# Kernel tuning notes

Hardware: AMD Instinct MI355X
Metric: run time of the kernel (lower is better)

Reference implementation:

```python
import jax, jax.numpy as jnp
import numpy as np

B_SZ, N_IN, N_CTX, UNITS, RANK = 4096, 4096, 512, 4096, 256


def setup_inputs() -> dict:
    key = jax.random.key(0)
    ks = jax.random.split(key, 8)
    inputs = jax.random.normal(ks[0], (B_SZ, N_IN), dtype=jnp.float32)
    context = jax.random.normal(ks[1], (B_SZ, N_CTX), dtype=jnp.float32)
    # Orthogonal-ish init approximated by scaled normals (math-equivalent shapes)
    U = jax.random.normal(ks[2], (N_IN, RANK), dtype=jnp.float32) / np.sqrt(N_IN)
    S = jax.random.uniform(ks[3], (RANK,), dtype=jnp.float32, minval=0.5, maxval=1.5)
    V = jax.random.normal(ks[4], (UNITS, RANK), dtype=jnp.float32) / np.sqrt(UNITS)
    W = jax.random.normal(ks[5], (N_CTX, RANK), dtype=jnp.float32) / np.sqrt(N_CTX)
    B = jnp.zeros((RANK,), dtype=jnp.float32)
    bias = jnp.zeros((UNITS,), dtype=jnp.float32)
    return {"inputs": inputs, "context": context, "U": U, "S": S, "V": V, "W": W, "B": B, "bias": bias}


def reference(inputs, context, U, S, V, W, B, bias):
    # chi[b,r] = sigmoid(context @ W + B)
    chi = jax.nn.sigmoid(context @ W + B)                  # [B, R]
    # Original: kernel[b,n,m] = sum_r U[n,r]*S[r]*chi[b,r]*V[m,r];
    # out[b,m] = sum_n x[b,n]*kernel[b,n,m]. Algebraically equal to:
    t = (inputs @ U) * (S * chi)                           # [B, R]
    out = t @ V.T + bias                                   # first '+ self.bias'
    out = out + bias                                       # 'outputs += self.bias' (use_bias=True)
    return jax.nn.relu(out)
```

## Files before the change

kernel.cpp:

```cpp
#include <hip/hip_runtime.h>

#define B_SZ 4096
#define N_IN 4096
#define N_CTX 512
#define UNITS 4096
#define RANK 256

typedef __attribute__((ext_vector_type(8))) __bf16 bf16x8;
typedef __attribute__((ext_vector_type(4))) float f32x4;
typedef __attribute__((ext_vector_type(8))) unsigned short ushort8;
typedef __attribute__((ext_vector_type(4))) unsigned short ushort4v;

__device__ __forceinline__ unsigned short f2bf(float f) {
    unsigned int u = __float_as_uint(f);
    u += 0x7FFFu + ((u >> 16) & 1u);
    return (unsigned short)(u >> 16);
}
__device__ __forceinline__ float bf2f(unsigned short h) {
    return __uint_as_float(((unsigned int)h) << 16);
}
__device__ __forceinline__ void gload_lds16(const unsigned short* g, unsigned short* l) {
    __builtin_amdgcn_global_load_lds(
        (const __attribute__((address_space(1))) unsigned int*)g,
        (__attribute__((address_space(3))) unsigned int*)l, 16, 0, 0);
}
__device__ __forceinline__ bf16x8 ldfrag(const unsigned short* p) {
    ushort8 t = *(const ushort8*)p;
    return __builtin_bit_cast(bf16x8, t);
}

__global__ void convT_kernel(const float* __restrict__ src, unsigned short* __restrict__ dst,
                             int K, int N) {
    int idx = blockIdx.x * 256 + threadIdx.x;
    int n = idx / K, k = idx - n * K;
    dst[idx] = f2bf(src[k * N + n]);
}
__global__ void conv_kernel(const float* __restrict__ src, unsigned short* __restrict__ dst) {
    int i = blockIdx.x * 256 + threadIdx.x;
    float4 v = ((const float4*)src)[i];
    ushort4v r = { f2bf(v.x), f2bf(v.y), f2bf(v.z), f2bf(v.w) };
    ((ushort4v*)dst)[i] = r;
}

__launch_bounds__(256)
__global__ void k1_chi(const float* __restrict__ ctx, const unsigned short* __restrict__ WT,
                       const float* __restrict__ S, const float* __restrict__ Bb,
                       unsigned short* __restrict__ Schi) {
    __shared__ unsigned short As[64 * 32];
    __shared__ unsigned short Bs[64 * 32];
    int tid = threadIdx.x, w = tid >> 6, lane = tid & 63;
    int ln15 = lane & 15, quad = lane >> 4;
    int wr = w >> 1, wc = w & 1;
    int tm = blockIdx.y * 64, tn = blockIdx.x * 64;
    f32x4 acc[2][2] = {};
    int arow = tid >> 2, ac8 = (tid & 3) * 8;
    const float* ag = ctx + (size_t)(tm + arow) * N_CTX + ac8;
    int brow = (w << 4) + (lane >> 2), bc8 = (lane & 3) * 8;
    const unsigned short* bg = WT + (size_t)(tn + brow) * N_CTX + bc8;
    unsigned short* bl = Bs + brow * 32 + bc8;
    for (int k0 = 0; k0 < N_CTX; k0 += 32) {
        gload_lds16(bg + k0, bl);
        float4 v0 = *(const float4*)(ag + k0);
        float4 v1 = *(const float4*)(ag + k0 + 4);
        ushort8 a8 = { f2bf(v0.x), f2bf(v0.y), f2bf(v0.z), f2bf(v0.w),
                       f2bf(v1.x), f2bf(v1.y), f2bf(v1.z), f2bf(v1.w) };
        *(ushort8*)(As + tid * 8) = a8;
        __syncthreads();
        bf16x8 af[2], bfr[2];
        for (int i = 0; i < 2; i++) af[i]  = ldfrag(As + (wr * 32 + i * 16 + ln15) * 32 + quad * 8);
        for (int j = 0; j < 2; j++) bfr[j] = ldfrag(Bs + (wc * 32 + j * 16 + ln15) * 32 + quad * 8);
        for (int i = 0; i < 2; i++)
            for (int j = 0; j < 2; j++)
                acc[i][j] = __builtin_amdgcn_mfma_f32_16x16x32_bf16(af[i], bfr[j], acc[i][j], 0, 0, 0);
        __syncthreads();
    }
    for (int j = 0; j < 2; j++) {
        int col = tn + wc * 32 + j * 16 + ln15;
        float sv = S[col], bv = Bb[col];
        for (int i = 0; i < 2; i++)
            for (int r = 0; r < 4; r++) {
                int row = tm + wr * 32 + i * 16 + quad * 4 + r;
                float x = acc[i][j][r] + bv;
                float chi = sv / (1.f + __expf(-x));
                Schi[(size_t)row * RANK + col] = f2bf(chi);
            }
    }
}

__launch_bounds__(256)
__global__ void k2_t0(const float* __restrict__ X, const unsigned short* __restrict__ UT,
                      float* __restrict__ T0) {
    __shared__ unsigned short As[128 * 32];
    __shared__ unsigned short Bs[128 * 32];
    int tid = threadIdx.x, w = tid >> 6, lane = tid & 63;
    int ln15 = lane & 15, quad = lane >> 4;
    int wr = w >> 1, wc = w & 1;
    int tn = blockIdx.x * 128, tm = blockIdx.y * 128;
    int kbase = blockIdx.z * 512;
    f32x4 acc[4][4] = {};
    int arow = tid >> 2, ac8 = (tid & 3) * 8;
    const float* ag0 = X + (size_t)(tm + arow) * N_IN + kbase + ac8;
    const float* ag1 = ag0 + (size_t)64 * N_IN;
    int bq = lane >> 2, bc8 = (lane & 3) * 8;
    for (int kt = 0; kt < 16; kt++) {
        int k0 = kt * 32;
        for (int ib = 0; ib < 2; ib++) {
            int row = (w << 5) + (ib << 4) + bq;
            gload_lds16(UT + (size_t)(tn + row) * N_IN + kbase + k0 + bc8, Bs + row * 32 + bc8);
        }
        {
            float4 v0 = *(const float4*)(ag0 + k0);
            float4 v1 = *(const float4*)(ag0 + k0 + 4);
            ushort8 a8 = { f2bf(v0.x), f2bf(v0.y), f2bf(v0.z), f2bf(v0.w),
                           f2bf(v1.x), f2bf(v1.y), f2bf(v1.z), f2bf(v1.w) };
            *(ushort8*)(As + tid * 8) = a8;
            float4 u0 = *(const float4*)(ag1 + k0);
            float4 u1 = *(const float4*)(ag1 + k0 + 4);
            ushort8 b8 = { f2bf(u0.x), f2bf(u0.y), f2bf(u0.z), f2bf(u0.w),
                           f2bf(u1.x), f2bf(u1.y), f2bf(u1.z), f2bf(u1.w) };
            *(ushort8*)(As + 2048 + tid * 8) = b8;
        }
        __syncthreads();
        bf16x8 af[4], bfr[4];
        for (int i = 0; i < 4; i++) af[i]  = ldfrag(As + (wr * 64 + i * 16 + ln15) * 32 + quad * 8);
        for (int j = 0; j < 4; j++) bfr[j] = ldfrag(Bs + (wc * 64 + j * 16 + ln15) * 32 + quad * 8);
        for (int i = 0; i < 4; i++)
            for (int j = 0; j < 4; j++)
                acc[i][j] = __builtin_amdgcn_mfma_f32_16x16x32_bf16(af[i], bfr[j], acc[i][j], 0, 0, 0);
        __syncthreads();
    }
    for (int i = 0; i < 4; i++)
        for (int j = 0; j < 4; j++) {
            int col = tn + wc * 64 + j * 16 + ln15;
            for (int r = 0; r < 4; r++) {
                int row = tm + wr * 64 + i * 16 + quad * 4 + r;
                atomicAdd(&T0[(size_t)row * RANK + col], acc[i][j][r]);
            }
        }
}

__global__ void e_mul(const float* __restrict__ T0, const unsigned short* __restrict__ Schi,
                      unsigned short* __restrict__ T) {
    int i = blockIdx.x * 256 + threadIdx.x;
    float4 t0 = ((const float4*)T0)[i];
    ushort4v sc = ((const ushort4v*)Schi)[i];
    ushort4v r = { f2bf(t0.x * bf2f(sc.x)), f2bf(t0.y * bf2f(sc.y)),
                   f2bf(t0.z * bf2f(sc.z)), f2bf(t0.w * bf2f(sc.w)) };
    ((ushort4v*)T)[i] = r;
}

__launch_bounds__(256)
__global__ void k3_out(const unsigned short* __restrict__ T, const unsigned short* __restrict__ Vb,
                       const float* __restrict__ bias, float* __restrict__ out) {
    __shared__ unsigned short As[128 * 32];
    __shared__ unsigned short Bs[128 * 32];
    int tid = threadIdx.x, w = tid >> 6, lane = tid & 63;
    int ln15 = lane & 15, quad = lane >> 4;
    int wr = w >> 1, wc = w & 1;
    int tn = blockIdx.x * 128, tm = blockIdx.y * 128;
    f32x4 acc[4][4] = {};
    int bq = lane >> 2, c8 = (lane & 3) * 8;
    for (int kt = 0; kt < 8; kt++) {
        int k0 = kt * 32;
        for (int ib = 0; ib < 2; ib++) {
            int row = (w << 5) + (ib << 4) + bq;
            gload_lds16(T  + (size_t)(tm + row) * RANK + k0 + c8, As + row * 32 + c8);
            gload_lds16(Vb + (size_t)(tn + row) * RANK + k0 + c8, Bs + row * 32 + c8);
        }
        __syncthreads();
        bf16x8 af[4], bfr[4];
        for (int i = 0; i < 4; i++) af[i]  = ldfrag(As + (wr * 64 + i * 16 + ln15) * 32 + quad * 8);
        for (int j = 0; j < 4; j++) bfr[j] = ldfrag(Bs + (wc * 64 + j * 16 + ln15) * 32 + quad * 8);
        for (int i = 0; i < 4; i++)
            for (int j = 0; j < 4; j++)
                acc[i][j] = __builtin_amdgcn_mfma_f32_16x16x32_bf16(af[i], bfr[j], acc[i][j], 0, 0, 0);
        __syncthreads();
    }
    for (int j = 0; j < 4; j++) {
        int col = tn + wc * 64 + j * 16 + ln15;
        float bv = 2.f * bias[col];
        for (int i = 0; i < 4; i++)
            for (int r = 0; r < 4; r++) {
                int row = tm + wr * 64 + i * 16 + quad * 4 + r;
                float v = acc[i][j][r] + bv;
                out[(size_t)row * UNITS + col] = fmaxf(v, 0.f);
            }
    }
}

extern "C" void kernel_launch(void* const* d_in, const int* in_sizes, int n_in,
                              void* d_out, int out_size, void* d_ws, size_t ws_size,
                              hipStream_t stream) {
    (void)in_sizes; (void)n_in; (void)out_size; (void)ws_size;
    const float* inputs  = (const float*)d_in[0];
    const float* context = (const float*)d_in[1];
    const float* U       = (const float*)d_in[2];
    const float* S       = (const float*)d_in[3];
    const float* V       = (const float*)d_in[4];
    const float* W       = (const float*)d_in[5];
    const float* Bb      = (const float*)d_in[6];
    const float* bias    = (const float*)d_in[7];
    float* out = (float*)d_out;

    char* ws = (char*)d_ws;
    size_t o = 0;
    unsigned short* UT   = (unsigned short*)(ws + o); o += (size_t)RANK * N_IN * 2;
    unsigned short* WT   = (unsigned short*)(ws + o); o += (size_t)RANK * N_CTX * 2;
    unsigned short* Vb   = (unsigned short*)(ws + o); o += (size_t)UNITS * RANK * 2;
    unsigned short* Schi = (unsigned short*)(ws + o); o += (size_t)B_SZ * RANK * 2;
    float*          T0   = (float*)(ws + o);          o += (size_t)B_SZ * RANK * 4;
    unsigned short* T    = (unsigned short*)(ws + o); o += (size_t)B_SZ * RANK * 2;

    hipMemsetAsync(T0, 0, (size_t)B_SZ * RANK * sizeof(float), stream);

    convT_kernel<<<(RANK * N_IN) / 256, 256, 0, stream>>>(U, UT, N_IN, RANK);
    convT_kernel<<<(RANK * N_CTX) / 256, 256, 0, stream>>>(W, WT, N_CTX, RANK);
    conv_kernel<<<(UNITS * RANK) / (256 * 4), 256, 0, stream>>>(V, Vb);

    k1_chi<<<dim3(RANK / 64, B_SZ / 64), 256, 0, stream>>>(context, WT, S, Bb, Schi);
    k2_t0<<<dim3(RANK / 128, B_SZ / 128, 8), 256, 0, stream>>>(inputs, UT, T0);
    e_mul<<<(B_SZ * RANK) / (256 * 4), 256, 0, stream>>>(T0, Schi, T);
    k3_out<<<dim3(UNITS / 128, B_SZ / 128), 256, 0, stream>>>(T, Vb, bias, out);
}
```

Before: 207.9 us.

## Replace atomic split-K with bf16 partials, tiled transposes, and deeper K tiles

```diff
diff --git a/kernel.cpp b/kernel.cpp
--- a/kernel.cpp
+++ b/kernel.cpp
@@ -5,6 +5,7 @@
 #define N_CTX 512
 #define UNITS 4096
 #define RANK 256
+#define ZSPLIT 8
 
 typedef __attribute__((ext_vector_type(8))) __bf16 bf16x8;
 typedef __attribute__((ext_vector_type(4))) float f32x4;
@@ -29,12 +30,29 @@
     return __builtin_bit_cast(bf16x8, t);
 }
 
-__global__ void convT_kernel(const float* __restrict__ src, unsigned short* __restrict__ dst,
-                             int K, int N) {
-    int idx = blockIdx.x * 256 + threadIdx.x;
-    int n = idx / K, k = idx - n * K;
-    dst[idx] = f2bf(src[k * N + n]);
-}
+__global__ void transpose_cvt(const float* __restrict__ src, unsigned short* __restrict__ dst,
+                              int R, int C) {
+    __shared__ unsigned short t[64][66];
+    int rb = blockIdx.x * 64, cb = blockIdx.y * 64;
+    int tid = threadIdx.x;
+    int r = tid >> 4, c4 = (tid & 15) * 4;
+    for (int i = 0; i < 4; i++) {
+        float4 v = *(const float4*)(src + (size_t)(rb + r + i * 16) * C + cb + c4);
+        t[r + i * 16][c4 + 0] = f2bf(v.x);
+        t[r + i * 16][c4 + 1] = f2bf(v.y);
+        t[r + i * 16][c4 + 2] = f2bf(v.z);
+        t[r + i * 16][c4 + 3] = f2bf(v.w);
+    }
+    __syncthreads();
+    int c = tid >> 3, r8 = (tid & 7) * 8;
+    for (int j = 0; j < 2; j++) {
+        int cc = c + j * 32;
+        ushort8 o;
+        for (int k = 0; k < 8; k++) o[k] = t[r8 + k][cc];
+        *(ushort8*)(dst + (size_t)(cb + cc) * R + rb + r8) = o;
+    }
+}
+
 __global__ void conv_kernel(const float* __restrict__ src, unsigned short* __restrict__ dst) {
     int i = blockIdx.x * 256 + threadIdx.x;
     float4 v = ((const float4*)src)[i];
@@ -42,138 +60,146 @@
     ((ushort4v*)dst)[i] = r;
 }
 
-__launch_bounds__(256)
+__launch_bounds__(256, 4)
 __global__ void k1_chi(const float* __restrict__ ctx, const unsigned short* __restrict__ WT,
                        const float* __restrict__ S, const float* __restrict__ Bb,
                        unsigned short* __restrict__ Schi) {
-    __shared__ unsigned short As[64 * 32];
-    __shared__ unsigned short Bs[64 * 32];
+    __shared__ unsigned short As[32 * 64];
+    __shared__ unsigned short Bs[64 * 64];
     int tid = threadIdx.x, w = tid >> 6, lane = tid & 63;
     int ln15 = lane & 15, quad = lane >> 4;
     int wr = w >> 1, wc = w & 1;
-    int tm = blockIdx.y * 64, tn = blockIdx.x * 64;
-    f32x4 acc[2][2] = {};
-    int arow = tid >> 2, ac8 = (tid & 3) * 8;
-    const float* ag = ctx + (size_t)(tm + arow) * N_CTX + ac8;
-    int brow = (w << 4) + (lane >> 2), bc8 = (lane & 3) * 8;
-    const unsigned short* bg = WT + (size_t)(tn + brow) * N_CTX + bc8;
-    unsigned short* bl = Bs + brow * 32 + bc8;
-    for (int k0 = 0; k0 < N_CTX; k0 += 32) {
-        gload_lds16(bg + k0, bl);
-        float4 v0 = *(const float4*)(ag + k0);
-        float4 v1 = *(const float4*)(ag + k0 + 4);
-        ushort8 a8 = { f2bf(v0.x), f2bf(v0.y), f2bf(v0.z), f2bf(v0.w),
-                       f2bf(v1.x), f2bf(v1.y), f2bf(v1.z), f2bf(v1.w) };
-        *(ushort8*)(As + tid * 8) = a8;
-        __syncthreads();
-        bf16x8 af[2], bfr[2];
-        for (int i = 0; i < 2; i++) af[i]  = ldfrag(As + (wr * 32 + i * 16 + ln15) * 32 + quad * 8);
-        for (int j = 0; j < 2; j++) bfr[j] = ldfrag(Bs + (wc * 32 + j * 16 + ln15) * 32 + quad * 8);
-        for (int i = 0; i < 2; i++)
-            for (int j = 0; j < 2; j++)
-                acc[i][j] = __builtin_amdgcn_mfma_f32_16x16x32_bf16(af[i], bfr[j], acc[i][j], 0, 0, 0);
+    int tm = blockIdx.y * 32, tn = blockIdx.x * 64;
+    f32x4 acc2[2] = {};
+    int arow = tid >> 3, ac4 = (tid & 7) * 4;
+    const float* ag = ctx + (size_t)(tm + arow) * N_CTX + ac4;
+    int brow0 = w * 16, bl8 = lane >> 3, bk8 = (lane & 7) * 8;
+    for (int kt = 0; kt < 8; kt++) {
+        int k0 = kt * 64;
+        for (int c = 0; c < 2; c++) {
+            int row = brow0 + c * 8 + bl8;
+            gload_lds16(WT + (size_t)(tn + row) * N_CTX + k0 + bk8, Bs + row * 64 + bk8);
+        }
+        for (int i = 0; i < 2; i++) {
+            float4 v = *(const float4*)(ag + k0 + i * 32);
+            ushort4v a4 = { f2bf(v.x), f2bf(v.y), f2bf(v.z), f2bf(v.w) };
+            *(ushort4v*)(As + arow * 64 + ac4 + i * 32) = a4;
+        }
+        __syncthreads();
+        for (int kh = 0; kh < 2; kh++) {
+            bf16x8 af = ldfrag(As + (wr * 16 + ln15) * 64 + kh * 32 + quad * 8);
+            for (int j = 0; j < 2; j++) {
+                bf16x8 bfr = ldfrag(Bs + (wc * 32 + j * 16 + ln15) * 64 + kh * 32 + quad * 8);
+                acc2[j] = __builtin_amdgcn_mfma_f32_16x16x32_bf16(af, bfr, acc2[j], 0, 0, 0);
+            }
+        }
         __syncthreads();
     }
     for (int j = 0; j < 2; j++) {
         int col = tn + wc * 32 + j * 16 + ln15;
         float sv = S[col], bv = Bb[col];
-        for (int i = 0; i < 2; i++)
-            for (int r = 0; r < 4; r++) {
-                int row = tm + wr * 32 + i * 16 + quad * 4 + r;
-                float x = acc[i][j][r] + bv;
-                float chi = sv / (1.f + __expf(-x));
-                Schi[(size_t)row * RANK + col] = f2bf(chi);
-            }
-    }
-}
-
-__launch_bounds__(256)
+        for (int r = 0; r < 4; r++) {
+            int row = tm + wr * 16 + quad * 4 + r;
+            float x = acc2[j][r] + bv;
+            float chi = sv / (1.f + __expf(-x));
+            Schi[(size_t)row * RANK + col] = f2bf(chi);
+        }
+    }
+}
+
+__launch_bounds__(256, 4)
 __global__ void k2_t0(const float* __restrict__ X, const unsigned short* __restrict__ UT,
-                      float* __restrict__ T0) {
-    __shared__ unsigned short As[128 * 32];
-    __shared__ unsigned short Bs[128 * 32];
+                      unsigned short* __restrict__ T0p) {
+    __shared__ unsigned short As[64 * 64];
+    __shared__ unsigned short Bs[128 * 64];
     int tid = threadIdx.x, w = tid >> 6, lane = tid & 63;
     int ln15 = lane & 15, quad = lane >> 4;
     int wr = w >> 1, wc = w & 1;
-    int tn = blockIdx.x * 128, tm = blockIdx.y * 128;
-    int kbase = blockIdx.z * 512;
-    f32x4 acc[4][4] = {};
-    int arow = tid >> 2, ac8 = (tid & 3) * 8;
-    const float* ag0 = X + (size_t)(tm + arow) * N_IN + kbase + ac8;
-    const float* ag1 = ag0 + (size_t)64 * N_IN;
-    int bq = lane >> 2, bc8 = (lane & 3) * 8;
-    for (int kt = 0; kt < 16; kt++) {
-        int k0 = kt * 32;
-        for (int ib = 0; ib < 2; ib++) {
-            int row = (w << 5) + (ib << 4) + bq;
-            gload_lds16(UT + (size_t)(tn + row) * N_IN + kbase + k0 + bc8, Bs + row * 32 + bc8);
-        }
-        {
-            float4 v0 = *(const float4*)(ag0 + k0);
-            float4 v1 = *(const float4*)(ag0 + k0 + 4);
-            ushort8 a8 = { f2bf(v0.x), f2bf(v0.y), f2bf(v0.z), f2bf(v0.w),
-                           f2bf(v1.x), f2bf(v1.y), f2bf(v1.z), f2bf(v1.w) };
-            *(ushort8*)(As + tid * 8) = a8;
-            float4 u0 = *(const float4*)(ag1 + k0);
-            float4 u1 = *(const float4*)(ag1 + k0 + 4);
-            ushort8 b8 = { f2bf(u0.x), f2bf(u0.y), f2bf(u0.z), f2bf(u0.w),
-                           f2bf(u1.x), f2bf(u1.y), f2bf(u1.z), f2bf(u1.w) };
-            *(ushort8*)(As + 2048 + tid * 8) = b8;
-        }
-        __syncthreads();
-        bf16x8 af[4], bfr[4];
-        for (int i = 0; i < 4; i++) af[i]  = ldfrag(As + (wr * 64 + i * 16 + ln15) * 32 + quad * 8);
-        for (int j = 0; j < 4; j++) bfr[j] = ldfrag(Bs + (wc * 64 + j * 16 + ln15) * 32 + quad * 8);
-        for (int i = 0; i < 4; i++)
+    int tm = blockIdx.y * 64, tn = blockIdx.x * 128;
+    int kbase = blockIdx.z * (N_IN / ZSPLIT);
+    f32x4 acc[2][4] = {};
+    int arow = tid >> 2, ac4 = (tid & 3) * 4;
+    const float* ag = X + (size_t)(tm + arow) * N_IN + kbase + ac4;
+    int brow0 = w * 32, bl8 = lane >> 3, bk8 = (lane & 7) * 8;
+    for (int kt = 0; kt < (N_IN / ZSPLIT) / 64; kt++) {
+        int k0 = kt * 64;
+        for (int c = 0; c < 4; c++) {
+            int row = brow0 + c * 8 + bl8;
+            gload_lds16(UT + (size_t)(tn + row) * N_IN + kbase + k0 + bk8, Bs + row * 64 + bk8);
+        }
+        for (int i = 0; i < 4; i++) {
+            float4 v = *(const float4*)(ag + k0 + i * 16);
+            ushort4v a4 = { f2bf(v.x), f2bf(v.y), f2bf(v.z), f2bf(v.w) };
+            *(ushort4v*)(As + arow * 64 + ac4 + i * 16) = a4;
+        }
+        __syncthreads();
+        for (int kh = 0; kh < 2; kh++) {
+            bf16x8 af[2], bfr[4];
+            for (int i = 0; i < 2; i++)
+                af[i] = ldfrag(As + (wr * 32 + i * 16 + ln15) * 64 + kh * 32 + quad * 8);
             for (int j = 0; j < 4; j++)
-                acc[i][j] = __builtin_amdgcn_mfma_f32_16x16x32_bf16(af[i], bfr[j], acc[i][j], 0, 0, 0);
-        __syncthreads();
-    }
-    for (int i = 0; i < 4; i++)
+                bfr[j] = ldfrag(Bs + (wc * 64 + j * 16 + ln15) * 64 + kh * 32 + quad * 8);
+            for (int i = 0; i < 2; i++)
+                for (int j = 0; j < 4; j++)
+                    acc[i][j] = __builtin_amdgcn_mfma_f32_16x16x32_bf16(af[i], bfr[j], acc[i][j], 0, 0, 0);
+        }
+        __syncthreads();
+    }
+    unsigned short* P = T0p + (size_t)blockIdx.z * B_SZ * RANK;
+    for (int i = 0; i < 2; i++)
         for (int j = 0; j < 4; j++) {
             int col = tn + wc * 64 + j * 16 + ln15;
             for (int r = 0; r < 4; r++) {
-                int row = tm + wr * 64 + i * 16 + quad * 4 + r;
-                atomicAdd(&T0[(size_t)row * RANK + col], acc[i][j][r]);
+                int row = tm + wr * 32 + i * 16 + quad * 4 + r;
+                P[(size_t)row * RANK + col] = f2bf(acc[i][j][r]);
             }
         }
 }
 
-__global__ void e_mul(const float* __restrict__ T0, const unsigned short* __restrict__ Schi,
+__global__ void e_red(const unsigned short* __restrict__ T0p, const unsigned short* __restrict__ Schi,
                       unsigned short* __restrict__ T) {
     int i = blockIdx.x * 256 + threadIdx.x;
-    float4 t0 = ((const float4*)T0)[i];
-    ushort4v sc = ((const ushort4v*)Schi)[i];
-    ushort4v r = { f2bf(t0.x * bf2f(sc.x)), f2bf(t0.y * bf2f(sc.y)),
-                   f2bf(t0.z * bf2f(sc.z)), f2bf(t0.w * bf2f(sc.w)) };
-    ((ushort4v*)T)[i] = r;
-}
-
-__launch_bounds__(256)
+    const size_t stride = (size_t)B_SZ * RANK;
+    float a[8] = {};
+    for (int z = 0; z < ZSPLIT; z++) {
+        ushort8 p = *(const ushort8*)(T0p + z * stride + (size_t)i * 8);
+        for (int k = 0; k < 8; k++) a[k] += bf2f(p[k]);
+    }
+    ushort8 s = *(const ushort8*)(Schi + (size_t)i * 8);
+    ushort8 o;
+    for (int k = 0; k < 8; k++) o[k] = f2bf(a[k] * bf2f(s[k]));
+    *(ushort8*)(T + (size_t)i * 8) = o;
+}
+
+__launch_bounds__(256, 3)
 __global__ void k3_out(const unsigned short* __restrict__ T, const unsigned short* __restrict__ Vb,
                        const float* __restrict__ bias, float* __restrict__ out) {
-    __shared__ unsigned short As[128 * 32];
-    __shared__ unsigned short Bs[128 * 32];
+    __shared__ unsigned short As[128 * 64];
+    __shared__ unsigned short Bs[128 * 64];
     int tid = threadIdx.x, w = tid >> 6, lane = tid & 63;
     int ln15 = lane & 15, quad = lane >> 4;
     int wr = w >> 1, wc = w & 1;
     int tn = blockIdx.x * 128, tm = blockIdx.y * 128;
     f32x4 acc[4][4] = {};
-    int bq = lane >> 2, c8 = (lane & 3) * 8;
-    for (int kt = 0; kt < 8; kt++) {
-        int k0 = kt * 32;
-        for (int ib = 0; ib < 2; ib++) {
-            int row = (w << 5) + (ib << 4) + bq;
-            gload_lds16(T  + (size_t)(tm + row) * RANK + k0 + c8, As + row * 32 + c8);
-            gload_lds16(Vb + (size_t)(tn + row) * RANK + k0 + c8, Bs + row * 32 + c8);
-        }
-        __syncthreads();
-        bf16x8 af[4], bfr[4];
-        for (int i = 0; i < 4; i++) af[i]  = ldfrag(As + (wr * 64 + i * 16 + ln15) * 32 + quad * 8);
-        for (int j = 0; j < 4; j++) bfr[j] = ldfrag(Bs + (wc * 64 + j * 16 + ln15) * 32 + quad * 8);
-        for (int i = 0; i < 4; i++)
+    int row0 = w * 32, bl8 = lane >> 3, bk8 = (lane & 7) * 8;
+    for (int kt = 0; kt < RANK / 64; kt++) {
+        int k0 = kt * 64;
+        for (int c = 0; c < 4; c++) {
+            int row = row0 + c * 8 + bl8;
+            gload_lds16(T  + (size_t)(tm + row) * RANK + k0 + bk8, As + row * 64 + bk8);
+            gload_lds16(Vb + (size_t)(tn + row) * RANK + k0 + bk8, Bs + row * 64 + bk8);
+        }
+        __syncthreads();
+        for (int kh = 0; kh < 2; kh++) {
+            bf16x8 af[4], bfr[4];
+            for (int i = 0; i < 4; i++)
+                af[i] = ldfrag(As + (wr * 64 + i * 16 + ln15) * 64 + kh * 32 + quad * 8);
             for (int j = 0; j < 4; j++)
-                acc[i][j] = __builtin_amdgcn_mfma_f32_16x16x32_bf16(af[i], bfr[j], acc[i][j], 0, 0, 0);
+                bfr[j] = ldfrag(Bs + (wc * 64 + j * 16 + ln15) * 64 + kh * 32 + quad * 8);
+            for (int i = 0; i < 4; i++)
+                for (int j = 0; j < 4; j++)
+                    acc[i][j] = __builtin_amdgcn_mfma_f32_16x16x32_bf16(af[i], bfr[j], acc[i][j], 0, 0, 0);
+        }
         __syncthreads();
     }
     for (int j = 0; j < 4; j++) {
@@ -208,17 +234,15 @@
     unsigned short* WT   = (unsigned short*)(ws + o); o += (size_t)RANK * N_CTX * 2;
     unsigned short* Vb   = (unsigned short*)(ws + o); o += (size_t)UNITS * RANK * 2;
     unsigned short* Schi = (unsigned short*)(ws + o); o += (size_t)B_SZ * RANK * 2;
-    float*          T0   = (float*)(ws + o);          o += (size_t)B_SZ * RANK * 4;
     unsigned short* T    = (unsigned short*)(ws + o); o += (size_t)B_SZ * RANK * 2;
-
-    hipMemsetAsync(T0, 0, (size_t)B_SZ * RANK * sizeof(float), stream);
-
-    convT_kernel<<<(RANK * N_IN) / 256, 256, 0, stream>>>(U, UT, N_IN, RANK);
-    convT_kernel<<<(RANK * N_CTX) / 256, 256, 0, stream>>>(W, WT, N_CTX, RANK);
+    unsigned short* T0p  = (unsigned short*)(ws + o); o += (size_t)ZSPLIT * B_SZ * RANK * 2;
+
+    transpose_cvt<<<dim3(N_IN / 64, RANK / 64), 256, 0, stream>>>(U, UT, N_IN, RANK);
+    transpose_cvt<<<dim3(N_CTX / 64, RANK / 64), 256, 0, stream>>>(W, WT, N_CTX, RANK);
     conv_kernel<<<(UNITS * RANK) / (256 * 4), 256, 0, stream>>>(V, Vb);
 
-    k1_chi<<<dim3(RANK / 64, B_SZ / 64), 256, 0, stream>>>(context, WT, S, Bb, Schi);
-    k2_t0<<<dim3(RANK / 128, B_SZ / 128, 8), 256, 0, stream>>>(inputs, UT, T0);
-    e_mul<<<(B_SZ * RANK) / (256 * 4), 256, 0, stream>>>(T0, Schi, T);
+    k2_t0<<<dim3(RANK / 128, B_SZ / 64, ZSPLIT), 256, 0, stream>>>(inputs, UT, T0p);
+    k1_chi<<<dim3(RANK / 64, B_SZ / 32), 256, 0, stream>>>(context, WT, S, Bb, Schi);
+    e_red<<<(B_SZ * RANK) / (256 * 8), 256, 0, stream>>>(T0p, Schi, T);
     k3_out<<<dim3(UNITS / 128, B_SZ / 128), 256, 0, stream>>>(T, Vb, bias, out);
 }
```

New measurement: 185.6 us. 1.12x faster.
